# Kernel tuning notes

Hardware: AMD Instinct MI355X
Metric: run time of the kernel (lower is better)

Reference implementation:

```python
import jax, jax.numpy as jnp
import numpy as np

N = 50000   # nodes
E = 800000  # edges
F = 128     # input features
H = 128     # hidden channels
G = 64      # graphs in batch
C = 10      # classes
L_HID = 3   # residual hidden GCN blocks
EPS = 1e-5  # BatchNorm eps


def setup_inputs() -> dict:
    key = jax.random.key(0)
    ks = jax.random.split(key, 10)
    sc = lambda k, s: (jax.random.normal(k, s, jnp.float32) * 0.05)
    x = jax.random.normal(ks[0], (N, F), jnp.float32)
    edge_index = jax.random.randint(ks[1], (2, E), 0, N, dtype=jnp.int32)
    batch = jnp.sort(jax.random.randint(ks[2], (N,), 0, G, dtype=jnp.int32))
    return {
        "x": x, "edge_index": edge_index, "batch": batch,
        # initial GCN block
        "W0": sc(ks[3], (F, H)), "b0": jnp.zeros(H, jnp.float32),
        "g0": jnp.ones(H, jnp.float32), "be0": jnp.zeros(H, jnp.float32),
        # 3 residual GCN blocks (stacked)
        "Wh": sc(ks[4], (L_HID, H, H)), "bh": jnp.zeros((L_HID, H), jnp.float32),
        "gh": jnp.ones((L_HID, H), jnp.float32), "beh": jnp.zeros((L_HID, H), jnp.float32),
        "Rh": sc(ks[5], (L_HID, H, H)),  # residual Linear (no bias)
        # MLP head: Linear(H,H)+ReLU, Linear(H,C)
        "mW1": sc(ks[6], (H, H)), "mb1": jnp.zeros(H, jnp.float32),
        "mW2": sc(ks[7], (H, C)), "mb2": jnp.zeros(C, jnp.float32),
    }


def _gcn_norm(edge_index, n):
    # add self-loops + symmetric normalization, as in PyG GCNConv
    loop = jnp.arange(n, dtype=edge_index.dtype)
    src = jnp.concatenate([edge_index[0], loop])
    dst = jnp.concatenate([edge_index[1], loop])
    deg = jax.ops.segment_sum(jnp.ones_like(dst, jnp.float32), dst, num_segments=n)
    dinv = jnp.where(deg > 0, jax.lax.rsqrt(deg), 0.0)
    coef = dinv[src] * dinv[dst]  # [E+N]
    return src, dst, coef


def _gcn_conv(x, W, b, src, dst, coef, n):
    h = x @ W                                   # [N, H] linear first (PyG order)
    msg = h[src] * coef[:, None]                # gather + normalize  [E+N, H]
    agg = jax.ops.segment_sum(msg, dst, num_segments=n)  # scatter-add [N, H]
    return agg + b


def _bn_relu(h, gamma, beta):
    # BatchNorm1d in eval mode with running_mean=0, running_var=1
    inv = jax.lax.rsqrt(jnp.asarray(1.0 + EPS, h.dtype))
    return jax.nn.relu(h * inv * gamma + beta)  # dropout is identity in eval


def reference(x, edge_index, batch, W0, b0, g0, be0, Wh, bh, gh, beh, Rh, mW1, mb1, mW2, mb2):
    n = x.shape[0]
    src, dst, coef = _gcn_norm(edge_index, n)
    # initial block (no residual)
    h = _bn_relu(_gcn_conv(x, W0, b0, src, dst, coef, n), g0, be0)
    # residual hidden blocks
    for i in range(Wh.shape[0]):
        c = _gcn_conv(h, Wh[i], bh[i], src, dst, coef, n) + h @ Rh[i]
        h = _bn_relu(c, gh[i], beh[i])
    # global max pool over graphs in the batch
    pooled = jax.ops.segment_max(h, batch, num_segments=G)  # [G, H]
    # MLP head
    z = jax.nn.relu(pooled @ mW1 + mb1)
    return z @ mW2 + mb2  # [G, C]
```

## Files before the change

kernel.cpp:

```cpp
#include <hip/hip_runtime.h>
#include <cstdint>
#include <cstddef>

#define NN 50000
#define NE 800000
#define NEPAD (NE + 3 * NN)
#define HID 128
#define NGRAPH 64
#define NCLASS 10
#define LHID 3
#define NREP 8

#define ROWBLK 3125
#define ROWBLK_PAD 3128
#define GEMM_GRID 782
#define FILL_GRID 3125
#define FRONT_DEG 3125
#define FRONT_A 3125
#define FRONT_B 56
#define FRONT_GRID (FRONT_DEG + FRONT_A + FRONT_B)

static constexpr float BN_INV = 0.9999950000374996f;

typedef __attribute__((ext_vector_type(8))) __bf16 bf16x8;
typedef __attribute__((ext_vector_type(4))) float floatx4;


__device__ __forceinline__ unsigned int f32_to_bf16_rne(float f) {
    unsigned int u = __float_as_uint(f);
    return (u + 0x7FFFu + ((u >> 16) & 1u)) >> 16;
}
__device__ __forceinline__ float bf16_to_f32(unsigned int h) {
    return __uint_as_float(h << 16);
}
__device__ __forceinline__ void split2(float a, float b, unsigned int& hi,
                                       unsigned int& lo) {
    unsigned int h0 = f32_to_bf16_rne(a), h1 = f32_to_bf16_rne(b);
    unsigned int l0 = f32_to_bf16_rne(a - bf16_to_f32(h0));
    unsigned int l1 = f32_to_bf16_rne(b - bf16_to_f32(h1));
    hi = h0 | (h1 << 16);
    lo = l0 | (l1 << 16);
}

__device__ __forceinline__ void gl2lds16(const void* g, void* l) {
    __builtin_amdgcn_global_load_lds((__attribute__((address_space(1))) void*)g,
                                     (__attribute__((address_space(3))) void*)l,
                                     16, 0, 0);
}


__global__ void k_front(const float* __restrict__ x, unsigned short* __restrict__ xH,
                        unsigned short* __restrict__ xL,
                        const float* __restrict__ W0, const float* __restrict__ Wh,
                        const float* __restrict__ Rh, unsigned short* __restrict__ bH,
                        unsigned short* __restrict__ bL,
                        const int* __restrict__ ei, int* __restrict__ deg8,
                        int* __restrict__ eslot) {
    const int b = blockIdx.x;
    const int tid = threadIdx.x;
    if (b < FRONT_DEG) {
        int e = b * 256 + tid;
        int d = ei[NE + e];
        int rep = e & (NREP - 1);
        eslot[e] = atomicAdd(&deg8[rep * NN + d], 1);
    } else if (b < FRONT_DEG + FRONT_A) {
        int u = (b - FRONT_DEG) * 256 + tid;
        int lane = u & 63;
        int blk = u >> 6;
        int kblk = blk & 3;
        int rowBlock = blk >> 2;
        int m = rowBlock * 16 + (lane & 15);
        int k = kblk * 32 + (lane >> 4) * 8;
        const float4* p = (const float4*)&x[(size_t)m * 128 + k];
        float4 v0 = p[0];
        float4 v1 = p[1];
        float vals[8] = {v0.x, v0.y, v0.z, v0.w, v1.x, v1.y, v1.z, v1.w};
        union { unsigned int i[4]; uint4 v; } H, L;
#pragma unroll
        for (int j = 0; j < 4; ++j) split2(vals[2 * j], vals[2 * j + 1], H.i[j], L.i[j]);
        *(uint4*)&xH[(size_t)u * 8] = H.v;
        *(uint4*)&xL[(size_t)u * 8] = L.v;
    } else {
        int cb = b - FRONT_DEG - FRONT_A;
        int mat = cb >> 3;
        const float* src = (mat == 0) ? W0
                         : (mat <= 3) ? (Wh + (size_t)(mat - 1) * 16384)
                                      : (Rh + (size_t)(mat - 4) * 16384);
        int u = (cb & 7) * 256 + tid;
        int lane = u & 63;
        int blk = u >> 6;
        int kblk = blk & 3;
        int nb = blk >> 2;
        int n = nb * 16 + (lane & 15);
        int k = kblk * 32 + (lane >> 4) * 8;
        union { unsigned int i[4]; uint4 v; } H, L;
#pragma unroll
        for (int j = 0; j < 4; ++j) {
            float a = src[(size_t)(k + 2 * j) * 128 + n];
            float c = src[(size_t)(k + 2 * j + 1) * 128 + n];
            split2(a, c, H.i[j], L.i[j]);
        }
        size_t base = (size_t)mat * 16384 + (size_t)u * 8;
        *(uint4*)&bH[base] = H.v;
        *(uint4*)&bL[base] = L.v;
    }
}


__global__ void k_scan1(const int* __restrict__ deg8, int* __restrict__ degT,
                        int* __restrict__ degOff, float* __restrict__ dinv,
                        int* __restrict__ bsum) {
    __shared__ int s[256];
    int i = blockIdx.x * 256 + threadIdx.x;
    int dsum = 0;
    if (i < NN) {
        int off[NREP];
#pragma unroll
        for (int r = 0; r < NREP; ++r) {
            off[r] = dsum;
            dsum += deg8[r * NN + i];
        }
#pragma unroll
        for (int r = 0; r < NREP; ++r) degOff[i * NREP + r] = off[r];
        degT[i] = dsum;
        dinv[i] = rsqrtf((float)(dsum + 1));
    }
    s[threadIdx.x] = (dsum + 3) & ~3;
    __syncthreads();
    for (int o = 128; o > 0; o >>= 1) {
        if (threadIdx.x < o) s[threadIdx.x] += s[threadIdx.x + o];
        __syncthreads();
    }
    if (threadIdx.x == 0) bsum[blockIdx.x] = s[0];
}


__global__ void k_scan3(const int* __restrict__ degT, const int* __restrict__ bsum,
                        int* __restrict__ rowptr, int* __restrict__ col,
                        float* __restrict__ cfv) {
    __shared__ int s[256];
    __shared__ int offS;
    const int bid = blockIdx.x;
    s[threadIdx.x] = (threadIdx.x < bid) ? bsum[threadIdx.x] : 0;
    __syncthreads();
    for (int o = 128; o > 0; o >>= 1) {
        if (threadIdx.x < o) s[threadIdx.x] += s[threadIdx.x + o];
        __syncthreads();
    }
    if (threadIdx.x == 0) offS = s[0];
    __syncthreads();
    const int off = offS;
    __syncthreads();
    int i = bid * 256 + threadIdx.x;
    int d = (i < NN) ? degT[i] : 0;
    int v = (d + 3) & ~3;
    s[threadIdx.x] = v;
    __syncthreads();
    for (int o = 1; o < 256; o <<= 1) {
        int tv = (threadIdx.x >= o) ? s[threadIdx.x - o] : 0;
        __syncthreads();
        s[threadIdx.x] += tv;
        __syncthreads();
    }
    if (i < NN) {
        int rp = off + s[threadIdx.x] - v;
        rowptr[i] = rp;
        for (int p = rp + d; p < rp + v; ++p) { col[p] = 0; cfv[p] = 0.f; }
    }
}


template <int NB, bool FILL>
__global__ __launch_bounds__(256, 3) void k_gemm_mfma(
    const unsigned short* __restrict__ Ahi, const unsigned short* __restrict__ Alo,
    const unsigned short* __restrict__ B1hi, const unsigned short* __restrict__ B1lo,
    const unsigned short* __restrict__ B2hi, const unsigned short* __restrict__ B2lo,
    float* __restrict__ C1, float* __restrict__ C2,
    const int* __restrict__ ei, const int* __restrict__ rowptr,
    const int* __restrict__ eslot, const int* __restrict__ degOff,
    const float* __restrict__ dinv, int* __restrict__ col,
    float* __restrict__ cfv) {
    __shared__ unsigned short lds[(1 + 2 * NB) * 4096];
    if (FILL && blockIdx.x >= GEMM_GRID) {
        int e = (blockIdx.x - GEMM_GRID) * 256 + threadIdx.x;
        int s = ei[e];
        int d = ei[NE + e];
        int rep = e & (NREP - 1);
        int p = rowptr[d] + degOff[d * NREP + rep] + eslot[e];
        col[p] = s;
        cfv[p] = dinv[s];
        return;
    }
    unsigned short* AhiS = lds;
    unsigned short* AloS = lds + 2048;
    unsigned short* B1hiS = lds + 4096;
    unsigned short* B1loS = lds + 8192;
    unsigned short* B2hiS = lds + 12288;
    unsigned short* B2loS = lds + 16384;

    const int tid = threadIdx.x;
    const int wave = tid >> 6;
    const int lane = tid & 63;
    const int wm = wave & 1;
    const int wn = wave >> 1;
    const int rb0 = blockIdx.x * 4;

    floatx4 acc1[2][4], acc2[2][4];
    floatx4 zero = {0.f, 0.f, 0.f, 0.f};
#pragma unroll
    for (int i = 0; i < 2; ++i)
#pragma unroll
        for (int j = 0; j < 4; ++j) { acc1[i][j] = zero; if (NB == 2) acc2[i][j] = zero; }

    for (int kc = 0; kc < 4; ++kc) {
        const int nit = (NB == 2) ? 10 : 6;
#pragma unroll
        for (int it = 0; it < nit; ++it) {
            int i = it * 4 + wave;
            const unsigned short* src;
            unsigned short* dst;
            if (i < 4)       { src = Ahi  + ((size_t)(rb0 + i) * 4 + kc) * 512;       dst = AhiS  + i * 512; }
            else if (i < 8)  { int rb = i - 4;  src = Alo  + ((size_t)(rb0 + rb) * 4 + kc) * 512; dst = AloS  + rb * 512; }
            else if (i < 16) { int nb = i - 8;  src = B1hi + ((size_t)nb * 4 + kc) * 512;         dst = B1hiS + nb * 512; }
            else if (i < 24) { int nb = i - 16; src = B1lo + ((size_t)nb * 4 + kc) * 512;         dst = B1loS + nb * 512; }
            else if (i < 32) { int nb = i - 24; src = B2hi + ((size_t)nb * 4 + kc) * 512;         dst = B2hiS + nb * 512; }
            else             { int nb = i - 32; src = B2lo + ((size_t)nb * 4 + kc) * 512;         dst = B2loS + nb * 512; }
            gl2lds16(src + (size_t)lane * 8, dst);
        }
        __syncthreads();

        bf16x8 aH[2], aL[2], bH[4], bL[4];
#pragma unroll
        for (int t = 0; t < 2; ++t)
            aH[t] = *(const bf16x8*)(AhiS + (wm * 2 + t) * 512 + lane * 8);
#pragma unroll
        for (int t = 0; t < 4; ++t)
            bH[t] = *(const bf16x8*)(B1hiS + (wn * 4 + t) * 512 + lane * 8);
#pragma unroll
        for (int tm = 0; tm < 2; ++tm)
#pragma unroll
            for (int tn = 0; tn < 4; ++tn)
                acc1[tm][tn] = __builtin_amdgcn_mfma_f32_16x16x32_bf16(
                    aH[tm], bH[tn], acc1[tm][tn], 0, 0, 0);
#pragma unroll
        for (int t = 0; t < 4; ++t)
            bL[t] = *(const bf16x8*)(B1loS + (wn * 4 + t) * 512 + lane * 8);
#pragma unroll
        for (int tm = 0; tm < 2; ++tm)
#pragma unroll
            for (int tn = 0; tn < 4; ++tn)
                acc1[tm][tn] = __builtin_amdgcn_mfma_f32_16x16x32_bf16(
                    aH[tm], bL[tn], acc1[tm][tn], 0, 0, 0);
#pragma unroll
        for (int t = 0; t < 2; ++t)
            aL[t] = *(const bf16x8*)(AloS + (wm * 2 + t) * 512 + lane * 8);
#pragma unroll
        for (int tm = 0; tm < 2; ++tm)
#pragma unroll
            for (int tn = 0; tn < 4; ++tn)
                acc1[tm][tn] = __builtin_amdgcn_mfma_f32_16x16x32_bf16(
                    aL[tm], bH[tn], acc1[tm][tn], 0, 0, 0);
        if (NB == 2) {
#pragma unroll
            for (int t = 0; t < 4; ++t)
                bH[t] = *(const bf16x8*)(B2hiS + (wn * 4 + t) * 512 + lane * 8);
#pragma unroll
            for (int tm = 0; tm < 2; ++tm)
#pragma unroll
                for (int tn = 0; tn < 4; ++tn)
                    acc2[tm][tn] = __builtin_amdgcn_mfma_f32_16x16x32_bf16(
                        aH[tm], bH[tn], acc2[tm][tn], 0, 0, 0);
#pragma unroll
            for (int tm = 0; tm < 2; ++tm)
#pragma unroll
                for (int tn = 0; tn < 4; ++tn)
                    acc2[tm][tn] = __builtin_amdgcn_mfma_f32_16x16x32_bf16(
                        aL[tm], bH[tn], acc2[tm][tn], 0, 0, 0);
#pragma unroll
            for (int t = 0; t < 4; ++t)
                bL[t] = *(const bf16x8*)(B2loS + (wn * 4 + t) * 512 + lane * 8);
#pragma unroll
            for (int tm = 0; tm < 2; ++tm)
#pragma unroll
                for (int tn = 0; tn < 4; ++tn)
                    acc2[tm][tn] = __builtin_amdgcn_mfma_f32_16x16x32_bf16(
                        aH[tm], bL[tn], acc2[tm][tn], 0, 0, 0);
        }
        __syncthreads();
    }

    const int quad = lane >> 4;
    const int col0 = lane & 15;
    const int rowBase = blockIdx.x * 64 + wm * 32;
#pragma unroll
    for (int tm = 0; tm < 2; ++tm) {
#pragma unroll
        for (int tn = 0; tn < 4; ++tn) {
            int c = wn * 64 + tn * 16 + col0;
#pragma unroll
            for (int r = 0; r < 4; ++r) {
                int row = rowBase + tm * 16 + quad * 4 + r;
                if (row < NN) {
                    C1[(size_t)row * 128 + c] = acc1[tm][tn][r];
                    if (NB == 2) C2[(size_t)row * 128 + c] = acc2[tm][tn][r];
                }
            }
        }
    }
}


template <bool RES, bool LAST>
__global__ __launch_bounds__(1024) void k_spmm(const float* __restrict__ t,
                                               const float* __restrict__ r,
                                               const int* __restrict__ rowptr,
                                               const int* __restrict__ degT,
                                               const int* __restrict__ col,
                                               const float* __restrict__ cfv,
                                               const float* __restrict__ dinv,
                                               const float* __restrict__ bias,
                                               const float* __restrict__ gamma,
                                               const float* __restrict__ beta,
                                               unsigned short* __restrict__ hHi,
                                               unsigned short* __restrict__ hLo,
                                               const int* __restrict__ batch,
                                               float* __restrict__ pooled) {
    __shared__ unsigned short shH[16][136];
    __shared__ unsigned short shL[16][136];
    __shared__ float shP[16][64][2];
    const int lane = threadIdx.x & 63;
    const int wave = threadIdx.x >> 6;
    const int f = lane * 2;
    const int node = blockIdx.x * 16 + wave;

    const float2 bv = *(const float2*)&bias[f];
    const float2 gv = *(const float2*)&gamma[f];
    const float2 ev = *(const float2*)&beta[f];

    const int start = rowptr[node];
    const int cnt4 = (degT[node] + 3) >> 2;
    float ax = 0.f, ay = 0.f;
#pragma unroll 2
    for (int q = 0; q < cnt4; ++q) {
        int4 cs = *(const int4*)&col[start + q * 4];
        float4 wv = *(const float4*)&cfv[start + q * 4];
        float2 v0 = *(const float2*)&t[(size_t)cs.x * 128 + f];
        float2 v1 = *(const float2*)&t[(size_t)cs.y * 128 + f];
        float2 v2 = *(const float2*)&t[(size_t)cs.z * 128 + f];
        float2 v3 = *(const float2*)&t[(size_t)cs.w * 128 + f];
        ax = fmaf(wv.x, v0.x, ax); ay = fmaf(wv.x, v0.y, ay);
        ax = fmaf(wv.y, v1.x, ax); ay = fmaf(wv.y, v1.y, ay);
        ax = fmaf(wv.z, v2.x, ax); ay = fmaf(wv.z, v2.y, ay);
        ax = fmaf(wv.w, v3.x, ax); ay = fmaf(wv.w, v3.y, ay);
    }
    const float di = dinv[node];
    const float dii = di * di;
    float2 tv = *(const float2*)&t[(size_t)node * 128 + f];
    float cx = di * ax + dii * tv.x + bv.x;
    float cy = di * ay + dii * tv.y + bv.y;
    if (RES) {
        float2 rv = *(const float2*)&r[(size_t)node * 128 + f];
        cx += rv.x;
        cy += rv.y;
    }
    const float ox = fmaxf(cx * (BN_INV * gv.x) + ev.x, 0.f);
    const float oy = fmaxf(cy * (BN_INV * gv.y) + ev.y, 0.f);

    if (LAST) {
        bool uni = (batch[blockIdx.x * 16] == batch[blockIdx.x * 16 + 15]);
        if (uni) {
            shP[wave][lane][0] = ox;
            shP[wave][lane][1] = oy;
            __syncthreads();
            if (wave == 0) {
                float a = shP[0][lane][0], b = shP[0][lane][1];
#pragma unroll
                for (int w = 1; w < 16; ++w) {
                    a = fmaxf(a, shP[w][lane][0]);
                    b = fmaxf(b, shP[w][lane][1]);
                }
                int g = batch[blockIdx.x * 16];
                atomicMax((unsigned int*)&pooled[g * 128 + f], __float_as_uint(a));
                atomicMax((unsigned int*)&pooled[g * 128 + f + 1], __float_as_uint(b));
            }
        } else {
            int g = batch[node];
            atomicMax((unsigned int*)&pooled[g * 128 + f], __float_as_uint(ox));
            atomicMax((unsigned int*)&pooled[g * 128 + f + 1], __float_as_uint(oy));
        }
        return;
    }

    unsigned int H, L;
    split2(ox, oy, H, L);
    ((unsigned int*)&shH[wave][0])[lane] = H;
    ((unsigned int*)&shL[wave][0])[lane] = L;
    __syncthreads();

    const int u = threadIdx.x >> 6;
    const int l = threadIdx.x & 63;
    const int m = l & 15;
    const int kg = l >> 4;
    if (u < 4) {
        uint4 H4 = *(const uint4*)&shH[m][u * 32 + kg * 8];
        ((uint4*)hHi)[((size_t)blockIdx.x * 4 + u) * 64 + l] = H4;
    } else if (u < 8) {
        int uu = u - 4;
        uint4 L4 = *(const uint4*)&shL[m][uu * 32 + kg * 8];
        ((uint4*)hLo)[((size_t)blockIdx.x * 4 + uu) * 64 + l] = L4;
    }
}


__global__ void k_head(const float* __restrict__ pooled, const float* __restrict__ mW1,
                       const float* __restrict__ mb1, const float* __restrict__ mW2,
                       const float* __restrict__ mb2, float* __restrict__ out) {
    __shared__ float p[128];
    __shared__ float z[128];
    int g = blockIdx.x;
    int j = threadIdx.x;
    p[j] = pooled[g * 128 + j];
    __syncthreads();
    float a = mb1[j];
#pragma unroll 8
    for (int k = 0; k < 128; ++k) a += p[k] * mW1[k * 128 + j];
    z[j] = fmaxf(a, 0.f);
    __syncthreads();
    if (j < NCLASS) {
        float o = mb2[j];
#pragma unroll 8
        for (int k = 0; k < 128; ++k) o += z[k] * mW2[k * NCLASS + j];
        out[g * NCLASS + j] = o;
    }
}


extern "C" void kernel_launch(void* const* d_in, const int* in_sizes, int n_in,
                              void* d_out, int out_size, void* d_ws, size_t ws_size,
                              hipStream_t stream) {
    const float* x   = (const float*)d_in[0];
    const int*   ei  = (const int*)d_in[1];
    const int* batch = (const int*)d_in[2];
    const float* W0  = (const float*)d_in[3];
    const float* b0  = (const float*)d_in[4];
    const float* g0  = (const float*)d_in[5];
    const float* be0 = (const float*)d_in[6];
    const float* Wh  = (const float*)d_in[7];
    const float* bh  = (const float*)d_in[8];
    const float* gh  = (const float*)d_in[9];
    const float* beh = (const float*)d_in[10];
    const float* Rh  = (const float*)d_in[11];
    const float* mW1 = (const float*)d_in[12];
    const float* mb1 = (const float*)d_in[13];
    const float* mW2 = (const float*)d_in[14];
    const float* mb2 = (const float*)d_in[15];
    float* out = (float*)d_out;

    char* ws = (char*)d_ws;
    size_t off = 0;
    auto alloc = [&](size_t bytes) -> void* {
        void* p = ws + off;
        off += (bytes + 255) & ~(size_t)255;
        return p;
    };
    int*   deg8   = (int*)alloc((size_t)NREP * NN * 4);
    float* pooled = (float*)alloc((size_t)NGRAPH * HID * 4);
    size_t zspan = (size_t)((char*)pooled - (char*)deg8) + (size_t)NGRAPH * HID * 4;
    int*   degT   = (int*)alloc((size_t)NN * 4);
    int*   degOff = (int*)alloc((size_t)NN * NREP * 4);
    int*   rowptr = (int*)alloc((size_t)NN * 4);
    float* dinv   = (float*)alloc((size_t)NN * 4);
    int*   bsum   = (int*)alloc(256 * 4);
    int*   eslot  = (int*)alloc((size_t)NE * 4);
    int*   col    = (int*)alloc((size_t)NEPAD * 4);
    float* cfv    = (float*)alloc((size_t)NEPAD * 4);
    float* t      = (float*)alloc((size_t)NN * HID * 4);
    float* rbuf   = (float*)alloc((size_t)NN * HID * 4);
    const size_t ASZ = (size_t)ROWBLK_PAD * 4 * 512;
    unsigned short* xH = (unsigned short*)alloc(ASZ * 2);
    unsigned short* xL = (unsigned short*)alloc(ASZ * 2);
    unsigned short* hH0 = (unsigned short*)alloc(ASZ * 2);
    unsigned short* hL0 = (unsigned short*)alloc(ASZ * 2);
    unsigned short* hH1 = (unsigned short*)alloc(ASZ * 2);
    unsigned short* hL1 = (unsigned short*)alloc(ASZ * 2);
    unsigned short* bH = (unsigned short*)alloc((size_t)7 * 16384 * 2);
    unsigned short* bL = (unsigned short*)alloc((size_t)7 * 16384 * 2);

    hipMemsetAsync(deg8, 0, zspan, stream);

    k_front<<<FRONT_GRID, 256, 0, stream>>>(x, xH, xL, W0, Wh, Rh, bH, bL,
                                            ei, deg8, eslot);
    k_scan1<<<(NN + 255) / 256, 256, 0, stream>>>(deg8, degT, degOff, dinv, bsum);
    k_scan3<<<(NN + 255) / 256, 256, 0, stream>>>(degT, bsum, rowptr, col, cfv);

    k_gemm_mfma<1, true><<<GEMM_GRID + FILL_GRID, 256, 0, stream>>>(
        xH, xL, bH, bL, nullptr, nullptr, t, nullptr,
        ei, rowptr, eslot, degOff, dinv, col, cfv);

    const int spmmGrid = NN / 16;
    k_spmm<false, false><<<spmmGrid, 1024, 0, stream>>>(
        t, nullptr, rowptr, degT, col, cfv, dinv, b0, g0, be0, hH0, hL0,
        nullptr, nullptr);

    unsigned short* hh[2] = {hH0, hH1};
    unsigned short* hl[2] = {hL0, hL1};
    int cur = 0;
    for (int i = 0; i < LHID; ++i) {
        unsigned short* ih = hh[cur];
        unsigned short* il = hl[cur];
        unsigned short* oh = hh[cur ^ 1];
        unsigned short* ol = hl[cur ^ 1];
        const unsigned short* w1H = bH + (size_t)(1 + i) * 16384;
        const unsigned short* w1L = bL + (size_t)(1 + i) * 16384;
        const unsigned short* w2H = bH + (size_t)(4 + i) * 16384;
        const unsigned short* w2L = bL + (size_t)(4 + i) * 16384;
        k_gemm_mfma<2, false><<<GEMM_GRID, 256, 0, stream>>>(
            ih, il, w1H, w1L, w2H, w2L, t, rbuf,
            nullptr, nullptr, nullptr, nullptr, nullptr, nullptr, nullptr);
        if (i < LHID - 1)
            k_spmm<true, false><<<spmmGrid, 1024, 0, stream>>>(
                t, rbuf, rowptr, degT, col, cfv, dinv, bh + i * HID, gh + i * HID,
                beh + i * HID, oh, ol, nullptr, nullptr);
        else
            k_spmm<true, true><<<spmmGrid, 1024, 0, stream>>>(
                t, rbuf, rowptr, degT, col, cfv, dinv, bh + i * HID, gh + i * HID,
                beh + i * HID, nullptr, nullptr, batch, pooled);
        cur ^= 1;
    }

    k_head<<<NGRAPH, 128, 0, stream>>>(pooled, mW1, mb1, mW2, mb2, out);
}
```

Baseline: 503.7 us.

## Slice feature matrix into 16-column panels and drop precomputed edge coefficients

The GEMM now writes its output in eight column-slices of 16 floats per node, and the SpMM is rebuilt so each block handles one slice for 16 nodes. Each gather then reads a 64-byte row from a 3.2 MB slice that can stay cache-resident, rather than scattered 512-byte rows. The per-edge coefficient array is removed: weights come from dinv[col] at gather time, and padding is marked with col=-1. The cost is eight times more index reads and extra dinv lookups per edge, plus divergence from looping to the maximum degree within a wave.

```diff
diff --git a/kernel.cpp b/kernel.cpp
--- a/kernel.cpp
+++ b/kernel.cpp
@@ -19,6 +19,9 @@
 #define FRONT_A 3125
 #define FRONT_B 56
 #define FRONT_GRID (FRONT_DEG + FRONT_A + FRONT_B)
+
+#define SPMM_GRID (NN / 16 * 8)
+#define SLICE_STRIDE ((size_t)NN * 16)
 
 static constexpr float BN_INV = 0.9999950000374996f;
 
@@ -136,8 +139,7 @@
 
 
 __global__ void k_scan3(const int* __restrict__ degT, const int* __restrict__ bsum,
-                        int* __restrict__ rowptr, int* __restrict__ col,
-                        float* __restrict__ cfv) {
+                        int* __restrict__ rowptr, int* __restrict__ col) {
     __shared__ int s[256];
     __shared__ int offS;
     const int bid = blockIdx.x;
@@ -165,7 +167,7 @@
     if (i < NN) {
         int rp = off + s[threadIdx.x] - v;
         rowptr[i] = rp;
-        for (int p = rp + d; p < rp + v; ++p) { col[p] = 0; cfv[p] = 0.f; }
+        for (int p = rp + d; p < rp + v; ++p) col[p] = -1;
     }
 }
 
@@ -178,8 +180,7 @@
     float* __restrict__ C1, float* __restrict__ C2,
     const int* __restrict__ ei, const int* __restrict__ rowptr,
     const int* __restrict__ eslot, const int* __restrict__ degOff,
-    const float* __restrict__ dinv, int* __restrict__ col,
-    float* __restrict__ cfv) {
+    int* __restrict__ col) {
     __shared__ unsigned short lds[(1 + 2 * NB) * 4096];
     if (FILL && blockIdx.x >= GEMM_GRID) {
         int e = (blockIdx.x - GEMM_GRID) * 256 + threadIdx.x;
@@ -188,7 +189,6 @@
         int rep = e & (NREP - 1);
         int p = rowptr[d] + degOff[d * NREP + rep] + eslot[e];
         col[p] = s;
-        cfv[p] = dinv[s];
         return;
     }
     unsigned short* AhiS = lds;
@@ -297,12 +297,13 @@
 #pragma unroll
         for (int tn = 0; tn < 4; ++tn) {
             int c = wn * 64 + tn * 16 + col0;
+            size_t sb = (size_t)(c >> 4) * SLICE_STRIDE + (size_t)(c & 15);
 #pragma unroll
             for (int r = 0; r < 4; ++r) {
                 int row = rowBase + tm * 16 + quad * 4 + r;
                 if (row < NN) {
-                    C1[(size_t)row * 128 + c] = acc1[tm][tn][r];
-                    if (NB == 2) C2[(size_t)row * 128 + c] = acc2[tm][tn][r];
+                    C1[sb + (size_t)row * 16] = acc1[tm][tn][r];
+                    if (NB == 2) C2[sb + (size_t)row * 16] = acc2[tm][tn][r];
                 }
             }
         }
@@ -311,103 +312,94 @@
 
 
 template <bool RES, bool LAST>
-__global__ __launch_bounds__(1024) void k_spmm(const float* __restrict__ t,
-                                               const float* __restrict__ r,
-                                               const int* __restrict__ rowptr,
-                                               const int* __restrict__ degT,
-                                               const int* __restrict__ col,
-                                               const float* __restrict__ cfv,
-                                               const float* __restrict__ dinv,
-                                               const float* __restrict__ bias,
-                                               const float* __restrict__ gamma,
-                                               const float* __restrict__ beta,
-                                               unsigned short* __restrict__ hHi,
-                                               unsigned short* __restrict__ hLo,
-                                               const int* __restrict__ batch,
-                                               float* __restrict__ pooled) {
-    __shared__ unsigned short shH[16][136];
-    __shared__ unsigned short shL[16][136];
-    __shared__ float shP[16][64][2];
-    const int lane = threadIdx.x & 63;
-    const int wave = threadIdx.x >> 6;
-    const int f = lane * 2;
-    const int node = blockIdx.x * 16 + wave;
-
-    const float2 bv = *(const float2*)&bias[f];
-    const float2 gv = *(const float2*)&gamma[f];
-    const float2 ev = *(const float2*)&beta[f];
+__global__ __launch_bounds__(256, 4) void k_spmm(
+    const float* __restrict__ t, const float* __restrict__ r,
+    const int* __restrict__ rowptr, const int* __restrict__ degT,
+    const int* __restrict__ col, const float* __restrict__ dinv,
+    const float* __restrict__ bias, const float* __restrict__ gamma,
+    const float* __restrict__ beta, unsigned short* __restrict__ hHi,
+    unsigned short* __restrict__ hLo, const int* __restrict__ batch,
+    float* __restrict__ pooled) {
+    __shared__ float sh[16][17];
+    __shared__ float shP[4][16];
+    const int tid = threadIdx.x;
+    const int lane = tid & 63;
+    const int wave = tid >> 6;
+    const int s = blockIdx.x & 7;
+    const int nb = blockIdx.x >> 3;
+    const int g = lane >> 4;
+    const int fl = lane & 15;
+    const int m = wave * 4 + g;
+    const int node = nb * 16 + m;
+    const int f = s * 16 + fl;
+    const float* ts = t + (size_t)s * SLICE_STRIDE;
 
     const int start = rowptr[node];
     const int cnt4 = (degT[node] + 3) >> 2;
-    float ax = 0.f, ay = 0.f;
+    int cmax = max(cnt4, __shfl_xor(cnt4, 16));
+    cmax = max(cmax, __shfl_xor(cmax, 32));
+
+    float a0 = 0.f, a1 = 0.f;
 #pragma unroll 2
-    for (int q = 0; q < cnt4; ++q) {
-        int4 cs = *(const int4*)&col[start + q * 4];
-        float4 wv = *(const float4*)&cfv[start + q * 4];
-        float2 v0 = *(const float2*)&t[(size_t)cs.x * 128 + f];
-        float2 v1 = *(const float2*)&t[(size_t)cs.y * 128 + f];
-        float2 v2 = *(const float2*)&t[(size_t)cs.z * 128 + f];
-        float2 v3 = *(const float2*)&t[(size_t)cs.w * 128 + f];
-        ax = fmaf(wv.x, v0.x, ax); ay = fmaf(wv.x, v0.y, ay);
-        ax = fmaf(wv.y, v1.x, ax); ay = fmaf(wv.y, v1.y, ay);
-        ax = fmaf(wv.z, v2.x, ax); ay = fmaf(wv.z, v2.y, ay);
-        ax = fmaf(wv.w, v3.x, ax); ay = fmaf(wv.w, v3.y, ay);
+    for (int q = 0; q < cmax; ++q) {
+        const bool act = q < cnt4;
+        const int base = act ? (start + q * 4) : 0;
+        int4 cs = *(const int4*)&col[base];
+        if (!act) { cs.x = -1; cs.y = -1; cs.z = -1; cs.w = -1; }
+        const int i0 = max(cs.x, 0), i1 = max(cs.y, 0);
+        const int i2 = max(cs.z, 0), i3 = max(cs.w, 0);
+        const float w0 = (cs.x < 0) ? 0.f : dinv[i0];
+        const float w1 = (cs.y < 0) ? 0.f : dinv[i1];
+        const float w2 = (cs.z < 0) ? 0.f : dinv[i2];
+        const float w3 = (cs.w < 0) ? 0.f : dinv[i3];
+        a0 = fmaf(w0, ts[(size_t)i0 * 16 + fl], a0);
+        a1 = fmaf(w1, ts[(size_t)i1 * 16 + fl], a1);
+        a0 = fmaf(w2, ts[(size_t)i2 * 16 + fl], a0);
+        a1 = fmaf(w3, ts[(size_t)i3 * 16 + fl], a1);
     }
     const float di = dinv[node];
     const float dii = di * di;
-    float2 tv = *(const float2*)&t[(size_t)node * 128 + f];
-    float cx = di * ax + dii * tv.x + bv.x;
-    float cy = di * ay + dii * tv.y + bv.y;
-    if (RES) {
-        float2 rv = *(const float2*)&r[(size_t)node * 128 + f];
-        cx += rv.x;
-        cy += rv.y;
-    }
-    const float ox = fmaxf(cx * (BN_INV * gv.x) + ev.x, 0.f);
-    const float oy = fmaxf(cy * (BN_INV * gv.y) + ev.y, 0.f);
+    const float tv = ts[(size_t)node * 16 + fl];
+    float c = di * (a0 + a1) + dii * tv + bias[f];
+    if (RES) c += r[(size_t)s * SLICE_STRIDE + (size_t)node * 16 + fl];
+    const float o = fmaxf(c * (BN_INV * gamma[f]) + beta[f], 0.f);
 
     if (LAST) {
-        bool uni = (batch[blockIdx.x * 16] == batch[blockIdx.x * 16 + 15]);
+        bool uni = (batch[nb * 16] == batch[nb * 16 + 15]);
         if (uni) {
-            shP[wave][lane][0] = ox;
-            shP[wave][lane][1] = oy;
+            float v = fmaxf(o, __shfl_xor(o, 16));
+            v = fmaxf(v, __shfl_xor(v, 32));
+            if (g == 0) shP[wave][fl] = v;
             __syncthreads();
-            if (wave == 0) {
-                float a = shP[0][lane][0], b = shP[0][lane][1];
-#pragma unroll
-                for (int w = 1; w < 16; ++w) {
-                    a = fmaxf(a, shP[w][lane][0]);
-                    b = fmaxf(b, shP[w][lane][1]);
-                }
-                int g = batch[blockIdx.x * 16];
-                atomicMax((unsigned int*)&pooled[g * 128 + f], __float_as_uint(a));
-                atomicMax((unsigned int*)&pooled[g * 128 + f + 1], __float_as_uint(b));
+            if (tid < 16) {
+                float a = fmaxf(fmaxf(shP[0][tid], shP[1][tid]),
+                                fmaxf(shP[2][tid], shP[3][tid]));
+                int gr = batch[nb * 16];
+                atomicMax((unsigned int*)&pooled[gr * 128 + s * 16 + tid],
+                          __float_as_uint(a));
             }
         } else {
-            int g = batch[node];
-            atomicMax((unsigned int*)&pooled[g * 128 + f], __float_as_uint(ox));
-            atomicMax((unsigned int*)&pooled[g * 128 + f + 1], __float_as_uint(oy));
+            atomicMax((unsigned int*)&pooled[batch[node] * 128 + f],
+                      __float_as_uint(o));
         }
         return;
     }
 
-    unsigned int H, L;
-    split2(ox, oy, H, L);
-    ((unsigned int*)&shH[wave][0])[lane] = H;
-    ((unsigned int*)&shL[wave][0])[lane] = L;
-    __syncthreads();
-
-    const int u = threadIdx.x >> 6;
-    const int l = threadIdx.x & 63;
-    const int m = l & 15;
-    const int kg = l >> 4;
-    if (u < 4) {
-        uint4 H4 = *(const uint4*)&shH[m][u * 32 + kg * 8];
-        ((uint4*)hHi)[((size_t)blockIdx.x * 4 + u) * 64 + l] = H4;
-    } else if (u < 8) {
-        int uu = u - 4;
-        uint4 L4 = *(const uint4*)&shL[m][uu * 32 + kg * 8];
-        ((uint4*)hLo)[((size_t)blockIdx.x * 4 + uu) * 64 + l] = L4;
+    sh[m][fl] = o;
+    __syncthreads();
+    if (tid < 32) {
+        const int mm = tid & 15;
+        const int k8l = tid >> 4;
+        float v[8];
+#pragma unroll
+        for (int j = 0; j < 8; ++j) v[j] = sh[mm][k8l * 8 + j];
+        union { unsigned int i[4]; uint4 u; } H, L;
+#pragma unroll
+        for (int j = 0; j < 4; ++j) split2(v[2 * j], v[2 * j + 1], H.i[j], L.i[j]);
+        const size_t uidx =
+            (size_t)(nb * 4 + (s >> 1)) * 64 + (size_t)((s & 1) * 32 + tid);
+        ((uint4*)hHi)[uidx] = H.u;
+        ((uint4*)hLo)[uidx] = L.u;
     }
 }
 
@@ -473,7 +465,6 @@
     int*   bsum   = (int*)alloc(256 * 4);
     int*   eslot  = (int*)alloc((size_t)NE * 4);
     int*   col    = (int*)alloc((size_t)NEPAD * 4);
-    float* cfv    = (float*)alloc((size_t)NEPAD * 4);
     float* t      = (float*)alloc((size_t)NN * HID * 4);
     float* rbuf   = (float*)alloc((size_t)NN * HID * 4);
     const size_t ASZ = (size_t)ROWBLK_PAD * 4 * 512;
@@ -491,15 +482,14 @@
     k_front<<<FRONT_GRID, 256, 0, stream>>>(x, xH, xL, W0, Wh, Rh, bH, bL,
                                             ei, deg8, eslot);
     k_scan1<<<(NN + 255) / 256, 256, 0, stream>>>(deg8, degT, degOff, dinv, bsum);
-    k_scan3<<<(NN + 255) / 256, 256, 0, stream>>>(degT, bsum, rowptr, col, cfv);
+    k_scan3<<<(NN + 255) / 256, 256, 0, stream>>>(degT, bsum, rowptr, col);
 
     k_gemm_mfma<1, true><<<GEMM_GRID + FILL_GRID, 256, 0, stream>>>(
         xH, xL, bH, bL, nullptr, nullptr, t, nullptr,
-        ei, rowptr, eslot, degOff, dinv, col, cfv);
-
-    const int spmmGrid = NN / 16;
-    k_spmm<false, false><<<spmmGrid, 1024, 0, stream>>>(
-        t, nullptr, rowptr, degT, col, cfv, dinv, b0, g0, be0, hH0, hL0,
+        ei, rowptr, eslot, degOff, col);
+
+    k_spmm<false, false><<<SPMM_GRID, 256, 0, stream>>>(
+        t, nullptr, rowptr, degT, col, dinv, b0, g0, be0, hH0, hL0,
         nullptr, nullptr);
 
     unsigned short* hh[2] = {hH0, hH1};
@@ -516,14 +506,14 @@
         const unsigned short* w2L = bL + (size_t)(4 + i) * 16384;
         k_gemm_mfma<2, false><<<GEMM_GRID, 256, 0, stream>>>(
             ih, il, w1H, w1L, w2H, w2L, t, rbuf,
-            nullptr, nullptr, nullptr, nullptr, nullptr, nullptr, nullptr);
+            nullptr, nullptr, nullptr, nullptr, nullptr);
         if (i < LHID - 1)
-            k_spmm<true, false><<<spmmGrid, 1024, 0, stream>>>(
-                t, rbuf, rowptr, degT, col, cfv, dinv, bh + i * HID, gh + i * HID,
+            k_spmm<true, false><<<SPMM_GRID, 256, 0, stream>>>(
+                t, rbuf, rowptr, degT, col, dinv, bh + i * HID, gh + i * HID,
                 beh + i * HID, oh, ol, nullptr, nullptr);
         else
-            k_spmm<true, true><<<spmmGrid, 1024, 0, stream>>>(
-                t, rbuf, rowptr, degT, col, cfv, dinv, bh + i * HID, gh + i * HID,
+            k_spmm<true, true><<<SPMM_GRID, 256, 0, stream>>>(
+                t, rbuf, rowptr, degT, col, dinv, bh + i * HID, gh + i * HID,
                 beh + i * HID, nullptr, nullptr, batch, pooled);
         cur ^= 1;
     }
```

After: 579.7 us. +15.1%, slower.
